# Optimization experiments

Measured on AMD Instinct MI355X. Metric: run time of the kernel, lower is better.

The kernel has to match this reference:

```python
import jax, jax.numpy as jnp
import numpy as np

B, T, D, E, K = 4, 2048, 1024, 8, 2

def setup_inputs() -> dict:
    key = jax.random.key(0)
    ks = jax.random.split(key, 4)
    scale = 1.0 / np.sqrt(D)
    return {
        "input_feat": jax.random.normal(ks[0], (B, T, D), dtype=jnp.float32),
        "delta": jax.random.normal(ks[1], (B, T, D), dtype=jnp.float32),
        "gate_W": jax.random.normal(ks[2], (E, D), dtype=jnp.float32) * scale,
        "gate_b": jnp.zeros((E,), dtype=jnp.float32),
        "expert_W": jax.random.normal(ks[3], (E, D, D), dtype=jnp.float32) * scale,
        "expert_b": jnp.zeros((E, D), dtype=jnp.float32),
    }

def reference(input_feat, delta, gate_W, gate_b, expert_W, expert_b):
    # Gating: logits [B,T,E], top-k over experts, softmax over the k logits
    gate_logits = jnp.einsum("btd,ed->bte", input_feat, gate_W) + gate_b
    topk_vals, topk_idx = jax.lax.top_k(gate_logits, K)          # [B,T,K]
    topk_weights = jax.nn.softmax(topk_vals, axis=-1)            # [B,T,K]

    # Dense per-expert linear on delta: [B,T,D,E] (torch Linear: x @ W.T + b)
    expert_outputs = jnp.einsum("btd,efd->btfe", delta, expert_W) + expert_b.T

    # Gather top-k expert outputs and weighted-combine
    idx = jnp.broadcast_to(topk_idx[:, :, None, :], (B, T, D, K))
    topk_outputs = jnp.take_along_axis(expert_outputs, idx, axis=-1)  # [B,T,D,K]
    weighted_output = jnp.sum(topk_outputs * topk_weights[:, :, None, :], axis=-1)
    return weighted_output
```

## Files before the change

kernel.cpp:

```cpp
#include <hip/hip_runtime.h>
#include <stdint.h>

#define NTOK 8192
#define D 1024
#define E 8
#define BM 128
#define BN 64
#define BK 64

typedef __attribute__((ext_vector_type(8))) short short8;
typedef __attribute__((ext_vector_type(4))) float f32x4;

__device__ __forceinline__ ushort f2bf(float f) {
  uint32_t x = __float_as_uint(f);
  x += 0x7FFFu + ((x >> 16) & 1u);
  return (ushort)(x >> 16);
}

#define NW4 2097152
#define ND4 2097152
#define NO4 2097152
__global__ __launch_bounds__(256) void convert_zero_kernel(
    const float* __restrict__ expert_W, const float* __restrict__ delta,
    ushort* __restrict__ Wb, ushort* __restrict__ Db,
    float* __restrict__ out, int* __restrict__ cnt) {
  int i = blockIdx.x * 256 + threadIdx.x;
  if (i < E) cnt[i] = 0;
  if (i < NW4) {
    float4 v = ((const float4*)expert_W)[i];
    ushort4 u; u.x = f2bf(v.x); u.y = f2bf(v.y); u.z = f2bf(v.z); u.w = f2bf(v.w);
    ((ushort4*)Wb)[i] = u;
  } else if (i < NW4 + ND4) {
    int j = i - NW4;
    float4 v = ((const float4*)delta)[j];
    ushort4 u; u.x = f2bf(v.x); u.y = f2bf(v.y); u.z = f2bf(v.z); u.w = f2bf(v.w);
    ((ushort4*)Db)[j] = u;
  } else {
    int j = i - NW4 - ND4;
    ((float4*)out)[j] = (float4){0.f, 0.f, 0.f, 0.f};
  }
}

__global__ __launch_bounds__(256) void gate_topk_kernel(
    const float* __restrict__ x, const float* __restrict__ gW,
    const float* __restrict__ gb,
    int* __restrict__ idx01, float2* __restrict__ w01) {
  int wave = threadIdx.x >> 6;
  int lane = threadIdx.x & 63;
  int t = blockIdx.x * 4 + wave;

  const float4* xr = (const float4*)(x + (size_t)t * D) + lane * 4;
  float acc[E];
#pragma unroll
  for (int e = 0; e < E; ++e) acc[e] = 0.f;
#pragma unroll
  for (int q = 0; q < 4; ++q) {
    float4 xv = xr[q];
#pragma unroll
    for (int e = 0; e < E; ++e) {
      float4 wv = ((const float4*)(gW + e * D))[lane * 4 + q];
      acc[e] += xv.x * wv.x + xv.y * wv.y + xv.z * wv.z + xv.w * wv.w;
    }
  }
#pragma unroll
  for (int e = 0; e < E; ++e) {
    float v = acc[e];
#pragma unroll
    for (int off = 32; off > 0; off >>= 1) v += __shfl_xor(v, off, 64);
    acc[e] = v;
  }
  if (lane == 0) {
    float lg[E];
#pragma unroll
    for (int e = 0; e < E; ++e) lg[e] = acc[e] + gb[e];
    int i0 = 0; float v0 = lg[0];
#pragma unroll
    for (int e = 1; e < E; ++e) { if (lg[e] > v0) { v0 = lg[e]; i0 = e; } }
    int i1 = -1; float v1 = -1e30f;
#pragma unroll
    for (int e = 0; e < E; ++e) { if (e != i0 && lg[e] > v1) { v1 = lg[e]; i1 = e; } }
    float e1 = __expf(v1 - v0);
    float inv = 1.f / (1.f + e1);
    idx01[t] = i0 | (i1 << 16);
    w01[t] = make_float2(inv, e1 * inv);
  }
}

__global__ __launch_bounds__(256) void bin_kernel(
    const int* __restrict__ idx01, const float2* __restrict__ w01,
    int* __restrict__ cnt, int* __restrict__ list, float* __restrict__ wlist) {
  __shared__ int hist[E];
  __shared__ int base[E];
  int tid = threadIdx.x;
  int t = blockIdx.x * 256 + tid;
  if (tid < E) hist[tid] = 0;
  __syncthreads();

  int packed = idx01[t];
  float2 w = w01[t];
  int i0 = packed & 0xFFFF, i1 = packed >> 16;
  int r0 = atomicAdd(&hist[i0], 1);
  int r1 = atomicAdd(&hist[i1], 1);
  __syncthreads();
  if (tid < E) base[tid] = atomicAdd(&cnt[tid], hist[tid]);
  __syncthreads();

  int s0 = base[i0] + r0;
  list[i0 * NTOK + s0] = t; wlist[i0 * NTOK + s0] = w.x;
  int s1 = base[i1] + r1;
  list[i1 * NTOK + s1] = t; wlist[i1 * NTOK + s1] = w.y;
}

__global__ __launch_bounds__(256) void moe_gemm_kernel(
    const ushort* __restrict__ Db, const ushort* __restrict__ Wb,
    const float* __restrict__ eb, const int* __restrict__ cnt,
    const int* __restrict__ list, const float* __restrict__ wlist,
    float* __restrict__ out) {
  int bx = blockIdx.x;
  int mt = bx >> 7;
  int rem = bx & 127;
  int e = rem >> 4;
  int nt = rem & 15;
  int M = cnt[e];
  int m0 = mt * BM;
  if (m0 >= M) return;
  int n0 = nt * BN;

  __shared__ ushort As[BM * BK];
  __shared__ ushort Bs[BN * BK];

  int tid = threadIdx.x;
  int wave = tid >> 6;
  int lane = tid & 63;
  int wm = wave >> 1;
  int wn = wave & 1;
  const int c = lane & 15;
  const int q = lane >> 4;

  const int* listE = list + e * NTOK;

  int rloc = lane >> 3;
  int gglob = (lane & 7) ^ rloc;
  const ushort* aptr[4];
  ushort* alds[4];
#pragma unroll
  for (int p = 0; p < 4; ++p) {
    int r = m0 + wave * 32 + p * 8 + rloc;
    int tok = listE[r < M ? r : m0];
    aptr[p] = Db + (size_t)tok * D + gglob * 8;
    alds[p] = &As[(wave * 32 + p * 8) * BK];
  }
  const ushort* WbE = Wb + ((size_t)e << 20);
  const ushort* bptr[2];
  ushort* blds[2];
#pragma unroll
  for (int sub = 0; sub < 2; ++sub) {
    int row = n0 + wave * 16 + sub * 8 + rloc;
    bptr[sub] = WbE + (size_t)row * D + gglob * 8;
    blds[sub] = &Bs[(wave * 16 + sub * 8) * BK];
  }

  f32x4 acc[4][2];
#pragma unroll
  for (int i = 0; i < 4; ++i)
#pragma unroll
    for (int j = 0; j < 2; ++j)
      acc[i][j] = (f32x4){0.f, 0.f, 0.f, 0.f};

  for (int k0 = 0; k0 < D; k0 += BK) {
#pragma unroll
    for (int p = 0; p < 4; ++p)
      __builtin_amdgcn_global_load_lds(
          (const __attribute__((address_space(1))) void*)(aptr[p] + k0),
          (__attribute__((address_space(3))) void*)alds[p], 16, 0, 0);
#pragma unroll
    for (int sub = 0; sub < 2; ++sub)
      __builtin_amdgcn_global_load_lds(
          (const __attribute__((address_space(1))) void*)(bptr[sub] + k0),
          (__attribute__((address_space(3))) void*)blds[sub], 16, 0, 0);
    __syncthreads();

#pragma unroll
    for (int s = 0; s < 2; ++s) {
      int sw = (((s * 4 + q) ^ (c & 7)) * 8);
      short8 a[4], b[2];
#pragma unroll
      for (int i = 0; i < 4; ++i)
        a[i] = *(const short8*)&As[(wm * 64 + i * 16 + c) * BK + sw];
#pragma unroll
      for (int j = 0; j < 2; ++j)
        b[j] = *(const short8*)&Bs[(wn * 32 + j * 16 + c) * BK + sw];
#pragma unroll
      for (int i = 0; i < 4; ++i)
#pragma unroll
        for (int j = 0; j < 2; ++j)
          acc[i][j] = __builtin_amdgcn_mfma_f32_16x16x32_bf16(a[i], b[j], acc[i][j], 0, 0, 0);
    }
    __syncthreads();
  }

  float bias[2];
#pragma unroll
  for (int j = 0; j < 2; ++j)
    bias[j] = eb[e * D + n0 + wn * 32 + j * 16 + c];
  const float* wlE = wlist + e * NTOK;
#pragma unroll
  for (int i = 0; i < 4; ++i) {
#pragma unroll
    for (int r = 0; r < 4; ++r) {
      int m = m0 + wm * 64 + i * 16 + q * 4 + r;
      if (m < M) {
        int tok = listE[m];
        float w = wlE[m];
        float* orow = out + (size_t)tok * D + n0 + wn * 32 + c;
#pragma unroll
        for (int j = 0; j < 2; ++j)
          atomicAdd(&orow[j * 16], (acc[i][j][r] + bias[j]) * w);
      }
    }
  }
}

extern "C" void kernel_launch(void* const* d_in, const int* in_sizes, int n_in,
                              void* d_out, int out_size, void* d_ws, size_t ws_size,
                              hipStream_t stream) {
  const float* input_feat = (const float*)d_in[0];
  const float* delta      = (const float*)d_in[1];
  const float* gate_W     = (const float*)d_in[2];
  const float* gate_b     = (const float*)d_in[3];
  const float* expert_W   = (const float*)d_in[4];
  const float* expert_b   = (const float*)d_in[5];
  float* out = (float*)d_out;

  char* ws = (char*)d_ws;
  ushort* Wb    = (ushort*)ws;
  ushort* Db    = (ushort*)(ws + 16777216);
  char*   meta  = ws + 2 * 16777216;
  int*    cnt   = (int*)meta;
  int*    list  = (int*)(meta + 256);
  float*  wlist = (float*)(meta + 256 + NTOK * E * 4);
  int*    idx01 = (int*)(meta + 256 + 2 * NTOK * E * 4);
  float2* w01   = (float2*)(meta + 256 + 2 * NTOK * E * 4 + NTOK * 4);

  int total4 = NW4 + ND4 + NO4;
  convert_zero_kernel<<<total4 / 256, 256, 0, stream>>>(expert_W, delta, Wb, Db, out, cnt);
  gate_topk_kernel<<<NTOK / 4, 256, 0, stream>>>(input_feat, gate_W, gate_b, idx01, w01);
  bin_kernel<<<NTOK / 256, 256, 0, stream>>>(idx01, w01, cnt, list, wlist);
  moe_gemm_kernel<<<(NTOK / BM) * 128, 256, 0, stream>>>(
      Db, Wb, expert_b, cnt, list, wlist, out);
}
```

Baseline: 238.4 us.

## Replace fp32 atomic combine with fp16 slot writes and fuse gating with binning

The GEMM epilogue no longer does fp32 atomicAdd into a zeroed output. Each token's two expert contributions are stored as fp16 values in separate halves of the output buffer, chosen by a rank bit packed into the token list, and a new combine kernel sums them in place into fp32. This removes the zero-fill pass and the atomic traffic, and gating and binning are merged into one kernel to drop a launch and the intermediate arrays. In exchange it adds an extra read/write pass over the output, stores intermediates at fp16 precision, and does the per-block binning serially in one thread.

```diff
diff --git a/kernel.cpp b/kernel.cpp
--- a/kernel.cpp
+++ b/kernel.cpp
@@ -1,4 +1,5 @@
 #include <hip/hip_runtime.h>
+#include <hip/hip_fp16.h>
 #include <stdint.h>
 
 #define NTOK 8192
@@ -17,36 +18,43 @@
   return (ushort)(x >> 16);
 }
 
+__device__ __forceinline__ ushort f2h(float f) {
+  union { __half h; ushort u; } c;
+  c.h = __float2half(f);
+  return c.u;
+}
+__device__ __forceinline__ float h2f(ushort u) {
+  union { __half h; ushort u; } c;
+  c.u = u;
+  return __half2float(c.h);
+}
+
 #define NW4 2097152
 #define ND4 2097152
-#define NO4 2097152
-__global__ __launch_bounds__(256) void convert_zero_kernel(
+__global__ __launch_bounds__(256) void convert_kernel(
     const float* __restrict__ expert_W, const float* __restrict__ delta,
-    ushort* __restrict__ Wb, ushort* __restrict__ Db,
-    float* __restrict__ out, int* __restrict__ cnt) {
+    ushort* __restrict__ Wb, ushort* __restrict__ Db, int* __restrict__ cnt) {
   int i = blockIdx.x * 256 + threadIdx.x;
   if (i < E) cnt[i] = 0;
   if (i < NW4) {
     float4 v = ((const float4*)expert_W)[i];
     ushort4 u; u.x = f2bf(v.x); u.y = f2bf(v.y); u.z = f2bf(v.z); u.w = f2bf(v.w);
     ((ushort4*)Wb)[i] = u;
-  } else if (i < NW4 + ND4) {
+  } else {
     int j = i - NW4;
     float4 v = ((const float4*)delta)[j];
     ushort4 u; u.x = f2bf(v.x); u.y = f2bf(v.y); u.z = f2bf(v.z); u.w = f2bf(v.w);
     ((ushort4*)Db)[j] = u;
-  } else {
-    int j = i - NW4 - ND4;
-    ((float4*)out)[j] = (float4){0.f, 0.f, 0.f, 0.f};
-  }
-}
-
-__global__ __launch_bounds__(256) void gate_topk_kernel(
+  }
+}
+
+__global__ __launch_bounds__(256) void gatebin_kernel(
     const float* __restrict__ x, const float* __restrict__ gW,
-    const float* __restrict__ gb,
-    int* __restrict__ idx01, float2* __restrict__ w01) {
+    const float* __restrict__ gb, int* __restrict__ cnt,
+    int* __restrict__ list, float* __restrict__ wlist) {
   int wave = threadIdx.x >> 6;
   int lane = threadIdx.x & 63;
+  int tid = threadIdx.x;
   int t = blockIdx.x * 4 + wave;
 
   const float4* xr = (const float4*)(x + (size_t)t * D) + lane * 4;
@@ -69,6 +77,13 @@
     for (int off = 32; off > 0; off >>= 1) v += __shfl_xor(v, off, 64);
     acc[e] = v;
   }
+
+  __shared__ int sIdx[4];
+  __shared__ float2 sW[4];
+  __shared__ int hist[E];
+  __shared__ int base[E];
+  __shared__ int rofs[4][2];
+
   if (lane == 0) {
     float lg[E];
 #pragma unroll
@@ -81,34 +96,38 @@
     for (int e = 0; e < E; ++e) { if (e != i0 && lg[e] > v1) { v1 = lg[e]; i1 = e; } }
     float e1 = __expf(v1 - v0);
     float inv = 1.f / (1.f + e1);
-    idx01[t] = i0 | (i1 << 16);
-    w01[t] = make_float2(inv, e1 * inv);
-  }
-}
-
-__global__ __launch_bounds__(256) void bin_kernel(
-    const int* __restrict__ idx01, const float2* __restrict__ w01,
-    int* __restrict__ cnt, int* __restrict__ list, float* __restrict__ wlist) {
-  __shared__ int hist[E];
-  __shared__ int base[E];
-  int tid = threadIdx.x;
-  int t = blockIdx.x * 256 + tid;
+    sIdx[wave] = i0 | (i1 << 16);
+    sW[wave] = make_float2(inv, e1 * inv);
+  }
   if (tid < E) hist[tid] = 0;
   __syncthreads();
 
-  int packed = idx01[t];
-  float2 w = w01[t];
-  int i0 = packed & 0xFFFF, i1 = packed >> 16;
-  int r0 = atomicAdd(&hist[i0], 1);
-  int r1 = atomicAdd(&hist[i1], 1);
+  if (tid == 0) {
+#pragma unroll
+    for (int w4 = 0; w4 < 4; ++w4) {
+      int p = sIdx[w4];
+      rofs[w4][0] = hist[p & 0xFFFF]++;
+      rofs[w4][1] = hist[p >> 16]++;
+    }
+  }
   __syncthreads();
-  if (tid < E) base[tid] = atomicAdd(&cnt[tid], hist[tid]);
+  if (tid < E) base[tid] = hist[tid] ? atomicAdd(&cnt[tid], hist[tid]) : 0;
   __syncthreads();
 
-  int s0 = base[i0] + r0;
-  list[i0 * NTOK + s0] = t; wlist[i0 * NTOK + s0] = w.x;
-  int s1 = base[i1] + r1;
-  list[i1 * NTOK + s1] = t; wlist[i1 * NTOK + s1] = w.y;
+  if (tid == 0) {
+#pragma unroll
+    for (int w4 = 0; w4 < 4; ++w4) {
+      int p = sIdx[w4];
+      int tk = blockIdx.x * 4 + w4;
+      int e0 = p & 0xFFFF, e1 = p >> 16;
+      int s0 = base[e0] + rofs[w4][0];
+      list[e0 * NTOK + s0] = tk;
+      wlist[e0 * NTOK + s0] = sW[w4].x;
+      int s1 = base[e1] + rofs[w4][1];
+      list[e1 * NTOK + s1] = tk | 0x80000000;
+      wlist[e1 * NTOK + s1] = sW[w4].y;
+    }
+  }
 }
 
 __global__ __launch_bounds__(256) void moe_gemm_kernel(
@@ -146,7 +165,7 @@
 #pragma unroll
   for (int p = 0; p < 4; ++p) {
     int r = m0 + wave * 32 + p * 8 + rloc;
-    int tok = listE[r < M ? r : m0];
+    int tok = listE[r < M ? r : m0] & 0x7FFFFFFF;
     aptr[p] = Db + (size_t)tok * D + gglob * 8;
     alds[p] = &As[(wave * 32 + p * 8) * BK];
   }
@@ -204,21 +223,36 @@
   for (int j = 0; j < 2; ++j)
     bias[j] = eb[e * D + n0 + wn * 32 + j * 16 + c];
   const float* wlE = wlist + e * NTOK;
+  ushort* outh = (ushort*)out;
 #pragma unroll
   for (int i = 0; i < 4; ++i) {
 #pragma unroll
     for (int r = 0; r < 4; ++r) {
       int m = m0 + wm * 64 + i * 16 + q * 4 + r;
       if (m < M) {
-        int tok = listE[m];
+        int en = listE[m];
+        int tok = en & 0x7FFFFFFF;
+        int rank = ((unsigned)en) >> 31;
         float w = wlE[m];
-        float* orow = out + (size_t)tok * D + n0 + wn * 32 + c;
+        size_t bi = ((size_t)tok * D + n0 + wn * 32 + c) * 2 + rank;
 #pragma unroll
         for (int j = 0; j < 2; ++j)
-          atomicAdd(&orow[j * 16], (acc[i][j][r] + bias[j]) * w);
+          outh[bi + j * 32] = f2h((acc[i][j][r] + bias[j]) * w);
       }
     }
   }
+}
+
+#define NC4 2097152
+__global__ __launch_bounds__(256) void combine_kernel(float* __restrict__ out) {
+  int i = blockIdx.x * 256 + threadIdx.x;
+  uint4 v = ((const uint4*)out)[i];
+  float4 r;
+  r.x = h2f((ushort)(v.x & 0xFFFF)) + h2f((ushort)(v.x >> 16));
+  r.y = h2f((ushort)(v.y & 0xFFFF)) + h2f((ushort)(v.y >> 16));
+  r.z = h2f((ushort)(v.z & 0xFFFF)) + h2f((ushort)(v.z >> 16));
+  r.w = h2f((ushort)(v.w & 0xFFFF)) + h2f((ushort)(v.w >> 16));
+  ((float4*)out)[i] = r;
 }
 
 extern "C" void kernel_launch(void* const* d_in, const int* in_sizes, int n_in,
@@ -239,13 +273,10 @@
   int*    cnt   = (int*)meta;
   int*    list  = (int*)(meta + 256);
   float*  wlist = (float*)(meta + 256 + NTOK * E * 4);
-  int*    idx01 = (int*)(meta + 256 + 2 * NTOK * E * 4);
-  float2* w01   = (float2*)(meta + 256 + 2 * NTOK * E * 4 + NTOK * 4);
-
-  int total4 = NW4 + ND4 + NO4;
-  convert_zero_kernel<<<total4 / 256, 256, 0, stream>>>(expert_W, delta, Wb, Db, out, cnt);
-  gate_topk_kernel<<<NTOK / 4, 256, 0, stream>>>(input_feat, gate_W, gate_b, idx01, w01);
-  bin_kernel<<<NTOK / 256, 256, 0, stream>>>(idx01, w01, cnt, list, wlist);
+
+  convert_kernel<<<(NW4 + ND4) / 256, 256, 0, stream>>>(expert_W, delta, Wb, Db, cnt);
+  gatebin_kernel<<<NTOK / 4, 256, 0, stream>>>(input_feat, gate_W, gate_b, cnt, list, wlist);
   moe_gemm_kernel<<<(NTOK / BM) * 128, 256, 0, stream>>>(
       Db, Wb, expert_b, cnt, list, wlist, out);
-}
+  combine_kernel<<<NC4 / 256, 256, 0, stream>>>(out);
+}
```

Result: faster. 229.8 us (-3.6%).
